# Performance work log

Hardware: AMD Instinct MI355X
Metric: run time of the kernel (lower is better)

The kernel has to match this reference:

```python
import jax, jax.numpy as jnp
import numpy as np

IN, H, B = 1024, 1024, 8192
EPS = 1e-5

def _ln(x, g, b):
    mu = jnp.mean(x, axis=-1, keepdims=True)
    var = jnp.mean(jnp.square(x - mu), axis=-1, keepdims=True)
    return (x - mu) * jax.lax.rsqrt(var + EPS) * g + b

def setup_inputs() -> dict:
    key = jax.random.key(0)
    ks = jax.random.split(key, 6)
    inp = {
        "input": jax.random.normal(ks[0], (B, IN), dtype=jnp.float32),
        "h_prev": jax.random.normal(ks[1], (B, H), dtype=jnp.float32),
        "c_prev": jax.random.normal(ks[2], (B, H), dtype=jnp.float32),
        # Linear(in, 4H, bias=False) weights, stored [out, in] like torch
        "w_i": jax.random.normal(ks[3], (4 * H, IN), dtype=jnp.float32) / np.sqrt(IN),
        "w_h": jax.random.normal(ks[4], (4 * H, H), dtype=jnp.float32) / np.sqrt(H),
    }
    for name in ("ln_i", "ln_h", "ln_g", "ln_o", "ln_c"):
        inp[name + "_g"] = jnp.ones((H,), dtype=jnp.float32)
        inp[name + "_b"] = jnp.zeros((H,), dtype=jnp.float32)
    return inp

def reference(input, h_prev, c_prev, w_i, w_h,
              ln_i_g, ln_i_b, ln_h_g, ln_h_b, ln_g_g, ln_g_b,
              ln_o_g, ln_o_b, ln_c_g, ln_c_b):
    gi = input @ w_i.T            # [B, 4H]
    gh = h_prev @ w_h.T           # [B, 4H]
    i_i, i_f, i_gc, i_o = jnp.split(gi, 4, axis=-1)
    h_i, h_f, h_g, h_o = jnp.split(gh, 4, axis=-1)
    i_g = jax.nn.sigmoid(_ln(i_i + h_i, ln_i_g, ln_i_b))
    f_g = jax.nn.sigmoid(_ln(i_f + h_f, ln_h_g, ln_h_b))
    # NOTE: faithful to source bug — uses sigmoided i_g (not chunk i_gc) here
    g_g = jnp.tanh(_ln(i_g + h_g, ln_g_g, ln_g_b))
    o_g = jax.nn.sigmoid(_ln(i_o + h_o, ln_o_g, ln_o_b))
    c_new = _ln(f_g * c_prev + i_g * g_g, ln_c_g, ln_c_b)
    h_new = o_g * jnp.tanh(c_new)
    return (h_new, c_new)
```

## Files before the change

kernel.cpp:

```cpp
#include <hip/hip_runtime.h>
#include <hip/hip_bf16.h>

#define BATCH 8192
#define HDIM  1024
#define KDIM  2048
#define NDIM  4096

__device__ inline unsigned short f2bf(float x) {
    unsigned int u = __float_as_uint(x);
    unsigned int r = (u + 0x7fffu + ((u >> 16) & 1u)) >> 16;
    return (unsigned short)r;
}
__device__ inline float bf2f(unsigned short u) {
    return __uint_as_float((unsigned int)u << 16);
}

__global__ __launch_bounds__(256) void convert_kernel(
    const float* __restrict__ wi, const float* __restrict__ wh,
    const float* __restrict__ input, const float* __restrict__ h_prev,
    unsigned short* __restrict__ Wb, unsigned short* __restrict__ Xb)
{
    int idx = blockIdx.x * 256 + threadIdx.x;
    const int NW = NDIM * 512;
    float4 v;
    unsigned short* dst;
    if (idx < NW) {
        int n = idx >> 9;
        int k = (idx & 511) << 2;
        if (k < 1024) {
            if (n >= 2048 && n < 3072) v = make_float4(0.f, 0.f, 0.f, 0.f);
            else                       v = *(const float4*)(wi + (size_t)n * 1024 + k);
        } else {
            v = *(const float4*)(wh + (size_t)n * 1024 + (k - 1024));
        }
        dst = Wb + (size_t)n * KDIM + k;
    } else {
        int j = idx - NW;
        int r = j >> 9;
        int k = (j & 511) << 2;
        if (k < 1024) v = *(const float4*)(input  + (size_t)r * 1024 + k);
        else          v = *(const float4*)(h_prev + (size_t)r * 1024 + (k - 1024));
        dst = Xb + (size_t)r * KDIM + k;
    }
    ushort4 o;
    o.x = f2bf(v.x); o.y = f2bf(v.y); o.z = f2bf(v.z); o.w = f2bf(v.w);
    *(ushort4*)dst = o;
}

#define BM 256
#define BN 128
#define BK 64

typedef __attribute__((ext_vector_type(8))) short bf16x8;
typedef __attribute__((ext_vector_type(4))) float f32x4;

__global__ __launch_bounds__(512) void gemm_bt_kernel(
    const unsigned short* __restrict__ A,
    const unsigned short* __restrict__ Bw,
    unsigned short* __restrict__ G,
    int M)
{
    __shared__ unsigned short As[BM * BK];
    __shared__ unsigned short Bs[BN * BK];

    const int tid  = threadIdx.x;
    const int lane = tid & 63;
    const int wave = tid >> 6;

    const int bid = blockIdx.x;
    const int bm  = (bid >> 5) * BM;
    const int bn  = (bid & 31) * BN;

    f32x4 acc[4][4] = {};

    const int wm = (wave >> 1) * 64;
    const int wn = (wave & 1) * 64;

    const int srow = lane >> 3;
    const int c_sw = (lane & 7) ^ srow;

    int k0 = 0;
    if (bn >= 2048 && bn < 3072) k0 = 1024;

    for (; k0 < KDIM; k0 += BK) {
#pragma unroll
        for (int p = 0; p < 4; ++p) {
            const int rbase = wave * 32 + p * 8;
            const unsigned short* gA =
                A + (size_t)(bm + rbase + srow) * KDIM + k0 + c_sw * 8;
            __builtin_amdgcn_global_load_lds(
                (const __attribute__((address_space(1))) void*)gA,
                (__attribute__((address_space(3))) void*)&As[rbase * BK], 16, 0, 0);
        }
#pragma unroll
        for (int p = 0; p < 2; ++p) {
            const int rbase = wave * 16 + p * 8;
            const unsigned short* gB =
                Bw + (size_t)(bn + rbase + srow) * KDIM + k0 + c_sw * 8;
            __builtin_amdgcn_global_load_lds(
                (const __attribute__((address_space(1))) void*)gB,
                (__attribute__((address_space(3))) void*)&Bs[rbase * BK], 16, 0, 0);
        }
        __syncthreads();

#pragma unroll
        for (int kk = 0; kk < 2; ++kk) {
            bf16x8 af[4], bfr[4];
            const int cbase = kk * 4 + (lane >> 4);
#pragma unroll
            for (int i = 0; i < 4; ++i) {
                const int ra = wm + i * 16 + (lane & 15);
                af[i]  = *(const bf16x8*)&As[ra * BK + ((cbase ^ (ra & 7)) * 8)];
                const int rb = wn + i * 16 + (lane & 15);
                bfr[i] = *(const bf16x8*)&Bs[rb * BK + ((cbase ^ (rb & 7)) * 8)];
            }
#pragma unroll
            for (int i = 0; i < 4; ++i)
#pragma unroll
                for (int j = 0; j < 4; ++j)
                    acc[i][j] = __builtin_amdgcn_mfma_f32_16x16x32_bf16(
                        af[i], bfr[j], acc[i][j], 0, 0, 0);
        }
        __syncthreads();
    }

#pragma unroll
    for (int i = 0; i < 4; ++i) {
#pragma unroll
        for (int j = 0; j < 4; ++j) {
#pragma unroll
            for (int r = 0; r < 4; ++r) {
                int row = bm + wm + i * 16 + (lane >> 4) * 4 + r;
                int col = bn + wn + j * 16 + (lane & 15);
                G[(size_t)row * NDIM + col] = f2bf(acc[i][j][r]);
            }
        }
    }
}

__device__ inline float sigmoid_f(float x) { return 1.f / (1.f + __expf(-x)); }
__device__ inline float tanh_f(float x) { return 1.f - 2.f / (__expf(2.f * x) + 1.f); }

typedef __attribute__((ext_vector_type(8))) unsigned short us8;

__device__ inline void wstats(const float* x, float& mu, float& rs)
{
    float s = 0.f, q = 0.f;
#pragma unroll
    for (int e = 0; e < 16; ++e) { s += x[e]; q += x[e] * x[e]; }
#pragma unroll
    for (int o = 1; o < 64; o <<= 1) {
        s += __shfl_xor(s, o);
        q += __shfl_xor(q, o);
    }
    mu = s * (1.f / 1024.f);
    float var = q * (1.f / 1024.f) - mu * mu;
    rs = rsqrtf(var + 1e-5f);
}

#define LOADG16(dst, basep)                                            \
    _Pragma("unroll")                                                  \
    for (int j = 0; j < 2; ++j) {                                      \
        us8 t = *(const us8*)((basep) + j * 512 + cbase);              \
        _Pragma("unroll")                                              \
        for (int e = 0; e < 8; ++e) dst[j * 8 + e] = bf2f(t[e]);       \
    }

#define LOADF16(dst, basep)                                            \
    _Pragma("unroll")                                                  \
    for (int j = 0; j < 2; ++j) {                                      \
        float4 a = *(const float4*)((basep) + j * 512 + cbase);        \
        float4 b = *(const float4*)((basep) + j * 512 + cbase + 4);    \
        dst[j * 8 + 0] = a.x; dst[j * 8 + 1] = a.y;                    \
        dst[j * 8 + 2] = a.z; dst[j * 8 + 3] = a.w;                    \
        dst[j * 8 + 4] = b.x; dst[j * 8 + 5] = b.y;                    \
        dst[j * 8 + 6] = b.z; dst[j * 8 + 7] = b.w;                    \
    }

__global__ __launch_bounds__(256) void lstm_ew_kernel(
    const unsigned short* __restrict__ G,
    const float* __restrict__ c_prev,
    const float* __restrict__ p0g, const float* __restrict__ p0b,
    const float* __restrict__ p1g, const float* __restrict__ p1b,
    const float* __restrict__ p2g, const float* __restrict__ p2b,
    const float* __restrict__ p3g, const float* __restrict__ p3b,
    const float* __restrict__ p4g, const float* __restrict__ p4b,
    float* __restrict__ out_h, float* __restrict__ out_c,
    int row_base)
{
    const int lane  = threadIdx.x & 63;
    const int wave  = threadIdx.x >> 6;
    const int r     = blockIdx.x * 4 + wave;
    const int grow  = row_base + r;
    const int cbase = lane * 8;

    const unsigned short* Grow = G + (size_t)r * NDIM;

    float tmp[16], pg[16], pb[16];
    float ig[16], cm[16], og[16];
    float mu, rs;

    LOADG16(tmp, Grow);
    wstats(tmp, mu, rs);
    LOADF16(pg, p0g); LOADF16(pb, p0b);
#pragma unroll
    for (int e = 0; e < 16; ++e)
        ig[e] = sigmoid_f((tmp[e] - mu) * rs * pg[e] + pb[e]);

    LOADG16(tmp, Grow + 1024);
    wstats(tmp, mu, rs);
    LOADF16(pg, p1g); LOADF16(pb, p1b);
    LOADF16(cm, c_prev + (size_t)grow * HDIM);
#pragma unroll
    for (int e = 0; e < 16; ++e)
        cm[e] *= sigmoid_f((tmp[e] - mu) * rs * pg[e] + pb[e]);

    LOADG16(tmp, Grow + 2048);
#pragma unroll
    for (int e = 0; e < 16; ++e) tmp[e] += ig[e];
    wstats(tmp, mu, rs);
    LOADF16(pg, p2g); LOADF16(pb, p2b);
#pragma unroll
    for (int e = 0; e < 16; ++e)
        cm[e] += ig[e] * tanh_f((tmp[e] - mu) * rs * pg[e] + pb[e]);

    LOADG16(tmp, Grow + 3072);
    wstats(tmp, mu, rs);
    LOADF16(pg, p3g); LOADF16(pb, p3b);
#pragma unroll
    for (int e = 0; e < 16; ++e)
        og[e] = sigmoid_f((tmp[e] - mu) * rs * pg[e] + pb[e]);

    wstats(cm, mu, rs);
    LOADF16(pg, p4g); LOADF16(pb, p4b);
    float cn[16], hn[16];
#pragma unroll
    for (int e = 0; e < 16; ++e) {
        cn[e] = (cm[e] - mu) * rs * pg[e] + pb[e];
        hn[e] = og[e] * tanh_f(cn[e]);
    }

    float* oh = out_h + (size_t)grow * HDIM;
    float* oc = out_c + (size_t)grow * HDIM;
#pragma unroll
    for (int j = 0; j < 2; ++j) {
        *(float4*)(oh + j * 512 + cbase) =
            make_float4(hn[j*8+0], hn[j*8+1], hn[j*8+2], hn[j*8+3]);
        *(float4*)(oh + j * 512 + cbase + 4) =
            make_float4(hn[j*8+4], hn[j*8+5], hn[j*8+6], hn[j*8+7]);
        *(float4*)(oc + j * 512 + cbase) =
            make_float4(cn[j*8+0], cn[j*8+1], cn[j*8+2], cn[j*8+3]);
        *(float4*)(oc + j * 512 + cbase + 4) =
            make_float4(cn[j*8+4], cn[j*8+5], cn[j*8+6], cn[j*8+7]);
    }
}

extern "C" void kernel_launch(void* const* d_in, const int* in_sizes, int n_in,
                              void* d_out, int out_size, void* d_ws, size_t ws_size,
                              hipStream_t stream)
{
    const float* input  = (const float*)d_in[0];
    const float* h_prev = (const float*)d_in[1];
    const float* c_prev = (const float*)d_in[2];
    const float* w_i    = (const float*)d_in[3];
    const float* w_h    = (const float*)d_in[4];
    const float* lng[10];
    for (int i = 0; i < 10; ++i) lng[i] = (const float*)d_in[5 + i];

    unsigned short* Xb = (unsigned short*)d_ws;
    size_t xb_bytes = (size_t)BATCH * KDIM * 2;
    unsigned short* Wb = (unsigned short*)((char*)d_ws + xb_bytes);
    size_t wb_bytes = (size_t)NDIM * KDIM * 2;
    unsigned short* G = (unsigned short*)((char*)d_ws + xb_bytes + wb_bytes);

    size_t g_avail = (ws_size > xb_bytes + wb_bytes) ? (ws_size - xb_bytes - wb_bytes) : 0;
    long max_rows = (long)(g_avail / ((size_t)NDIM * sizeof(unsigned short)));
    int chunk = (max_rows >= BATCH) ? BATCH : (int)((max_rows / BM) * BM);
    if (chunk <= 0) chunk = BM;

    convert_kernel<<<(NDIM * 512 + BATCH * 512) / 256, 256, 0, stream>>>(
        w_i, w_h, input, h_prev, Wb, Xb);

    float* out_h = (float*)d_out;
    float* out_c = out_h + (size_t)BATCH * HDIM;

    for (int rb = 0; rb < BATCH; rb += chunk) {
        int rows = (BATCH - rb < chunk) ? (BATCH - rb) : chunk;
        gemm_bt_kernel<<<(rows / BM) * (NDIM / BN), 512, 0, stream>>>(
            Xb + (size_t)rb * KDIM, Wb, G, rows);
        lstm_ew_kernel<<<rows / 4, 256, 0, stream>>>(
            G, c_prev, lng[0], lng[1], lng[2], lng[3], lng[4],
            lng[5], lng[6], lng[7], lng[8], lng[9], out_h, out_c, rb);
    }
}
```

Measured before the change: 335.1 us.

## Switch GEMM to 32x32x16 MFMA and reorder block-to-tile mapping by N stripes

Replaces the 16x16x32 bf16 MFMA tiling (4x4 accumulators per wave) with 32x32x16 MFMA (2x2 accumulators of 16 floats), halving the LDS fragment loads per wave per K-step. It also changes the block index mapping so consecutive blocks walk down M within a stripe of 8 N-tiles, aiming for better L2 reuse of weight tiles. The epilogue index math is updated for the 32x32 output layout. This adds register pressure risk from the larger accumulators and may change LDS bank-conflict behaviour with the existing swizzle.

After: 366.3 us. +9.3%, slower.

```diff
diff --git a/kernel.cpp b/kernel.cpp
--- a/kernel.cpp
+++ b/kernel.cpp
@@ -52,7 +52,7 @@
 #define BK 64
 
 typedef __attribute__((ext_vector_type(8))) short bf16x8;
-typedef __attribute__((ext_vector_type(4))) float f32x4;
+typedef __attribute__((ext_vector_type(16))) float f32x16;
 
 __global__ __launch_bounds__(512) void gemm_bt_kernel(
     const unsigned short* __restrict__ A,
@@ -67,11 +67,14 @@
     const int lane = tid & 63;
     const int wave = tid >> 6;
 
-    const int bid = blockIdx.x;
-    const int bm  = (bid >> 5) * BM;
-    const int bn  = (bid & 31) * BN;
-
-    f32x4 acc[4][4] = {};
+    const int m_tiles = M / BM;
+    const int per_stripe = m_tiles * 8;
+    const int s   = blockIdx.x / per_stripe;
+    const int rem = blockIdx.x % per_stripe;
+    const int bm  = (rem >> 3) * BM;
+    const int bn  = ((s << 3) + (rem & 7)) * BN;
+
+    f32x16 acc[2][2] = {};
 
     const int wm = (wave >> 1) * 64;
     const int wn = (wave & 1) * 64;
@@ -104,35 +107,35 @@
         __syncthreads();
 
 #pragma unroll
-        for (int kk = 0; kk < 2; ++kk) {
-            bf16x8 af[4], bfr[4];
-            const int cbase = kk * 4 + (lane >> 4);
-#pragma unroll
-            for (int i = 0; i < 4; ++i) {
-                const int ra = wm + i * 16 + (lane & 15);
-                af[i]  = *(const bf16x8*)&As[ra * BK + ((cbase ^ (ra & 7)) * 8)];
-                const int rb = wn + i * 16 + (lane & 15);
-                bfr[i] = *(const bf16x8*)&Bs[rb * BK + ((cbase ^ (rb & 7)) * 8)];
+        for (int ks = 0; ks < 4; ++ks) {
+            const int kc = ks * 2 + (lane >> 5);
+            bf16x8 af[2], bfr[2];
+#pragma unroll
+            for (int mm = 0; mm < 2; ++mm) {
+                const int ra = wm + mm * 32 + (lane & 31);
+                af[mm]  = *(const bf16x8*)&As[ra * BK + ((kc ^ (ra & 7)) * 8)];
+                const int rb = wn + mm * 32 + (lane & 31);
+                bfr[mm] = *(const bf16x8*)&Bs[rb * BK + ((kc ^ (rb & 7)) * 8)];
             }
 #pragma unroll
-            for (int i = 0; i < 4; ++i)
-#pragma unroll
-                for (int j = 0; j < 4; ++j)
-                    acc[i][j] = __builtin_amdgcn_mfma_f32_16x16x32_bf16(
-                        af[i], bfr[j], acc[i][j], 0, 0, 0);
+            for (int mm = 0; mm < 2; ++mm)
+#pragma unroll
+                for (int nn = 0; nn < 2; ++nn)
+                    acc[mm][nn] = __builtin_amdgcn_mfma_f32_32x32x16_bf16(
+                        af[mm], bfr[nn], acc[mm][nn], 0, 0, 0);
         }
         __syncthreads();
     }
 
 #pragma unroll
-    for (int i = 0; i < 4; ++i) {
-#pragma unroll
-        for (int j = 0; j < 4; ++j) {
-#pragma unroll
-            for (int r = 0; r < 4; ++r) {
-                int row = bm + wm + i * 16 + (lane >> 4) * 4 + r;
-                int col = bn + wn + j * 16 + (lane & 15);
-                G[(size_t)row * NDIM + col] = f2bf(acc[i][j][r]);
+    for (int mm = 0; mm < 2; ++mm) {
+#pragma unroll
+        for (int nn = 0; nn < 2; ++nn) {
+#pragma unroll
+            for (int r = 0; r < 16; ++r) {
+                int row = bm + wm + mm * 32 + (r & 3) + 8 * (r >> 2) + 4 * (lane >> 5);
+                int col = bn + wn + nn * 32 + (lane & 31);
+                G[(size_t)row * NDIM + col] = f2bf(acc[mm][nn][r]);
             }
         }
     }
```
